# Performance work log

Measured on AMD Instinct MI355X. Metric: run time of the kernel, lower is better.

Reference implementation:

```python
import jax, jax.numpy as jnp
import numpy as np

B, C, H, W = 16, 64, 64, 64
HEADS = 8

def conv1x1(x, w):
    # x: [B, Cin, H, W], w: [Cout, Cin] -> [B, Cout, H, W]
    return jnp.einsum('oc,bchw->bohw', w, x)

def maxpool2x2(x):
    b, c, h, w = x.shape
    return x.reshape(b, c, h // 2, 2, w // 2, 2).max(axis=(3, 5))

def setup_inputs() -> dict:
    key = jax.random.key(0)
    ks = jax.random.split(key, 6)
    x = jax.random.normal(ks[0], (B, C, H, W), dtype=jnp.float32)
    w_theta = jax.random.normal(ks[1], (C // HEADS, C), dtype=jnp.float32) * 0.05
    w_phi = jax.random.normal(ks[2], (C // HEADS, C), dtype=jnp.float32) * 0.05
    w_g = jax.random.normal(ks[3], (C // 2, C), dtype=jnp.float32) * 0.05
    w_o = jax.random.normal(ks[4], (C, C // 2), dtype=jnp.float32) * 0.05
    gamma = jax.random.normal(ks[5], (), dtype=jnp.float32)
    return {'x': x, 'w_theta': w_theta, 'w_phi': w_phi, 'w_g': w_g, 'w_o': w_o, 'gamma': gamma}

def reference(x, w_theta, w_phi, w_g, w_o, gamma):
    b, c, h, w = x.shape
    n = h * w                      # query length
    m = n // 4                     # kv length after 2x2 maxpool
    theta = conv1x1(x, w_theta).reshape(b, c // HEADS, n)   # [B, C/h, N]
    phi = maxpool2x2(conv1x1(x, w_phi)).reshape(b, c // HEADS, m)  # [B, C/h, M]
    g = maxpool2x2(conv1x1(x, w_g)).reshape(b, c // 2, m)   # [B, C/2, M]
    # attention: theta^T @ phi -> [B, N, M]; NOTE: no 1/sqrt(d) scaling (SAGAN)
    beta = jax.nn.softmax(jnp.einsum('bdn,bdm->bnm', theta, phi), axis=-1)
    # o = g @ beta^T -> [B, C/2, N]
    o = jnp.einsum('bdm,bnm->bdn', g, beta).reshape(b, c // 2, h, w)
    o = conv1x1(o, w_o)            # [B, C, H, W]
    return gamma * o + x
```

## Files before the change

kernel.cpp:

```cpp
#include <hip/hip_runtime.h>
#include <hip/hip_bf16.h>

#define NB 16
#define NC 64
#define NN 4096
#define NM 1024
#define ND 8
#define NG 32

typedef short short8 __attribute__((ext_vector_type(8)));
typedef float floatx4 __attribute__((ext_vector_type(4)));
typedef float floatx2 __attribute__((ext_vector_type(2)));

#define LOG2E 1.44269504f

__device__ __forceinline__ short f2bfs(float f) {
    union { __hip_bfloat16 h; short s; } u;
    u.h = __float2bfloat16(f);
    return u.s;
}
__device__ __forceinline__ unsigned pack2bf(float a, float b) {
    return (unsigned)(unsigned short)f2bfs(a) | ((unsigned)(unsigned short)f2bfs(b) << 16);
}
__device__ __forceinline__ unsigned pk2fast(float a, float b) {
    unsigned ua = __float_as_uint(a) + 0x8000u;
    unsigned ub = __float_as_uint(b) + 0x8000u;
    return __builtin_amdgcn_perm(ub, ua, 0x07060302);
}
__device__ __forceinline__ float bflo(unsigned u) { return __uint_as_float(u << 16); }
__device__ __forceinline__ float bfhi(unsigned u) { return __uint_as_float(u & 0xffff0000u); }
__device__ __forceinline__ floatx2 fma2(floatx2 a, float b, floatx2 c) {
    return __builtin_elementwise_fma(a, (floatx2)(b), c);
}

__global__ __launch_bounds__(256)
void proj_kernel(const float* __restrict__ x,
                 const float* __restrict__ w_theta,
                 const float* __restrict__ w_phi,
                 const float* __restrict__ w_g,
                 const float* __restrict__ w_o,
                 unsigned* __restrict__ theta_ws,
                 unsigned* __restrict__ phi_ws,
                 unsigned* __restrict__ g2_ws)
{
    __shared__ __align__(16) float xl[64 * 128];
    __shared__ float lwt[512];
    __shared__ float lwp[512];
    __shared__ float lwg[2048];
    __shared__ float lwo[2048];
    __shared__ __align__(16) float lgs[32 * 36];
    __shared__ float lps[32 * 8];

    const int b  = blockIdx.x >> 5;
    const int ph = blockIdx.x & 31;
    const int t  = threadIdx.x;

    for (int i = t; i < 512;  i += 256) { lwt[i] = w_theta[i]; lwp[i] = w_phi[i]; }
    for (int i = t; i < 2048; i += 256) { lwg[i] = w_g[i];     lwo[i] = w_o[i]; }

    const float* xb = x + (size_t)b * NC * NN + (size_t)ph * 128;
    for (int idx = t; idx < 2048; idx += 256) {
        int c = idx >> 5, i4 = idx & 31;
        ((float4*)xl)[c * 32 + i4] = ((const float4*)(xb + (size_t)c * NN))[i4];
    }
    __syncthreads();

    if (t < 128) {
        float th[8];
        #pragma unroll
        for (int oc = 0; oc < 8; ++oc) th[oc] = 0.f;
        for (int c = 0; c < 64; ++c) {
            float xv = xl[c * 128 + t];
            #pragma unroll
            for (int oc = 0; oc < 8; ++oc) th[oc] = fmaf(lwt[oc * 64 + c], xv, th[oc]);
        }
        uint4 pk;
        pk.x = pack2bf(th[0] * LOG2E, th[1] * LOG2E);
        pk.y = pack2bf(th[2] * LOG2E, th[3] * LOG2E);
        pk.z = pack2bf(th[4] * LOG2E, th[5] * LOG2E);
        pk.w = pack2bf(th[6] * LOG2E, th[7] * LOG2E);
        ((uint4*)theta_ws)[(size_t)b * NN + ph * 128 + t] = pk;

        int m = t >> 2, oc0 = (t & 3) * 2;
        float s[2][4];
        #pragma unroll
        for (int a = 0; a < 2; ++a)
            #pragma unroll
            for (int p = 0; p < 4; ++p) s[a][p] = 0.f;
        #pragma unroll 4
        for (int c = 0; c < 64; ++c) {
            const float* xr = &xl[c * 128];
            float x0 = xr[2 * m], x1 = xr[2 * m + 1], x2 = xr[64 + 2 * m], x3 = xr[65 + 2 * m];
            #pragma unroll
            for (int a = 0; a < 2; ++a) {
                float w = lwp[(oc0 + a) * 64 + c];
                s[a][0] = fmaf(w, x0, s[a][0]);
                s[a][1] = fmaf(w, x1, s[a][1]);
                s[a][2] = fmaf(w, x2, s[a][2]);
                s[a][3] = fmaf(w, x3, s[a][3]);
            }
        }
        #pragma unroll
        for (int a = 0; a < 2; ++a)
            lps[m * 8 + oc0 + a] = fmaxf(fmaxf(s[a][0], s[a][1]), fmaxf(s[a][2], s[a][3]));
    } else {
        int tt = t - 128;
        int oc0 = (tt >> 3) * 2, grp = tt & 7;
        float s0[16], s1[16];
        #pragma unroll
        for (int i = 0; i < 16; ++i) { s0[i] = 0.f; s1[i] = 0.f; }
        const float4* xl4 = (const float4*)xl;
        #pragma unroll 2
        for (int c = 0; c < 64; ++c) {
            float4 a0 = xl4[c * 32 + 2 * grp];
            float4 a1 = xl4[c * 32 + 2 * grp + 1];
            float4 b0 = xl4[c * 32 + 16 + 2 * grp];
            float4 b1 = xl4[c * 32 + 17 + 2 * grp];
            float w0 = lwg[oc0 * 64 + c], w1 = lwg[(oc0 + 1) * 64 + c];
            s0[0] = fmaf(w0, a0.x, s0[0]);  s0[1] = fmaf(w0, a0.y, s0[1]);
            s0[2] = fmaf(w0, a0.z, s0[2]);  s0[3] = fmaf(w0, a0.w, s0[3]);
            s0[4] = fmaf(w0, a1.x, s0[4]);  s0[5] = fmaf(w0, a1.y, s0[5]);
            s0[6] = fmaf(w0, a1.z, s0[6]);  s0[7] = fmaf(w0, a1.w, s0[7]);
            s0[8] = fmaf(w0, b0.x, s0[8]);  s0[9] = fmaf(w0, b0.y, s0[9]);
            s0[10] = fmaf(w0, b0.z, s0[10]); s0[11] = fmaf(w0, b0.w, s0[11]);
            s0[12] = fmaf(w0, b1.x, s0[12]); s0[13] = fmaf(w0, b1.y, s0[13]);
            s0[14] = fmaf(w0, b1.z, s0[14]); s0[15] = fmaf(w0, b1.w, s0[15]);
            s1[0] = fmaf(w1, a0.x, s1[0]);  s1[1] = fmaf(w1, a0.y, s1[1]);
            s1[2] = fmaf(w1, a0.z, s1[2]);  s1[3] = fmaf(w1, a0.w, s1[3]);
            s1[4] = fmaf(w1, a1.x, s1[4]);  s1[5] = fmaf(w1, a1.y, s1[5]);
            s1[6] = fmaf(w1, a1.z, s1[6]);  s1[7] = fmaf(w1, a1.w, s1[7]);
            s1[8] = fmaf(w1, b0.x, s1[8]);  s1[9] = fmaf(w1, b0.y, s1[9]);
            s1[10] = fmaf(w1, b0.z, s1[10]); s1[11] = fmaf(w1, b0.w, s1[11]);
            s1[12] = fmaf(w1, b1.x, s1[12]); s1[13] = fmaf(w1, b1.y, s1[13]);
            s1[14] = fmaf(w1, b1.z, s1[14]); s1[15] = fmaf(w1, b1.w, s1[15]);
        }
        #pragma unroll
        for (int p = 0; p < 4; ++p) {
            float v0 = fmaxf(fmaxf(s0[2 * p], s0[2 * p + 1]), fmaxf(s0[8 + 2 * p], s0[9 + 2 * p]));
            float v1 = fmaxf(fmaxf(s1[2 * p], s1[2 * p + 1]), fmaxf(s1[8 + 2 * p], s1[9 + 2 * p]));
            lgs[oc0 * 36 + grp * 4 + p]       = v0;
            lgs[(oc0 + 1) * 36 + grp * 4 + p] = v1;
        }
    }
    __syncthreads();

    {
        int co = t >> 2, m0 = (t & 3) * 8;
        float v[8];
        #pragma unroll
        for (int mm = 0; mm < 8; ++mm) v[mm] = 0.f;
        #pragma unroll 4
        for (int c = 0; c < 32; ++c) {
            float w = lwo[co * 32 + c];
            float4 ga = ((const float4*)&lgs[c * 36 + m0])[0];
            float4 gb = ((const float4*)&lgs[c * 36 + m0])[1];
            v[0] = fmaf(w, ga.x, v[0]); v[1] = fmaf(w, ga.y, v[1]);
            v[2] = fmaf(w, ga.z, v[2]); v[3] = fmaf(w, ga.w, v[3]);
            v[4] = fmaf(w, gb.x, v[4]); v[5] = fmaf(w, gb.y, v[5]);
            v[6] = fmaf(w, gb.z, v[6]); v[7] = fmaf(w, gb.w, v[7]);
        }
        uint4 pk;
        pk.x = pack2bf(v[0], v[1]); pk.y = pack2bf(v[2], v[3]);
        pk.z = pack2bf(v[4], v[5]); pk.w = pack2bf(v[6], v[7]);
        int lane = ((t & 3) << 4) | ((t >> 2) & 15);
        ((uint4*)g2_ws)[(((size_t)b * 4 + (t >> 6)) * 32 + ph) * 64 + lane] = pk;
    }

    if (t < 32) {
        const float* pr = &lps[t * 8];
        uint4 pk;
        pk.x = pack2bf(pr[0], pr[1]); pk.y = pack2bf(pr[2], pr[3]);
        pk.z = pack2bf(pr[4], pr[5]); pk.w = pack2bf(pr[6], pr[7]);
        ((uint4*)phi_ws)[(size_t)b * NM + ph * 32 + t] = pk;
    }
}

__global__ __launch_bounds__(256, 2)
void attn_kernel(const unsigned* __restrict__ theta_ws,
                 const unsigned* __restrict__ phi_ws,
                 const unsigned* __restrict__ g2_ws,
                 const float* __restrict__ gamma_p,
                 const float* __restrict__ x,
                 float* __restrict__ out)
{
    __shared__ __align__(16) float lphi[NM * 8 + 16];

    const int b    = blockIdx.x >> 5;
    const int qblk = blockIdx.x & 31;
    const int t    = threadIdx.x;
    const int w    = t >> 6;
    const int lane = t & 63;
    const int lm   = lane & 15;
    const int quad = lane >> 4;
    const int q0   = qblk * 128 + w * 32;

    for (int kk = t; kk < NM; kk += 256) {
        uint4 v = ((const uint4*)phi_ws)[(size_t)b * NM + kk];
        float* dst = lphi + kk * 8 + ((kk >> 3) & 3) * 4;
        ((float4*)dst)[0] = make_float4(bflo(v.x), bfhi(v.x), bflo(v.y), bfhi(v.y));
        ((float4*)dst)[1] = make_float4(bflo(v.z), bfhi(v.z), bflo(v.w), bfhi(v.w));
    }

    floatx2 th2[8];
    {
        uint4 v0 = ((const uint4*)theta_ws)[(size_t)b * NN + q0 + lm];
        uint4 v1 = ((const uint4*)theta_ws)[(size_t)b * NN + q0 + 16 + lm];
        th2[0] = floatx2{bflo(v0.x), bflo(v1.x)}; th2[1] = floatx2{bfhi(v0.x), bfhi(v1.x)};
        th2[2] = floatx2{bflo(v0.y), bflo(v1.y)}; th2[3] = floatx2{bfhi(v0.y), bfhi(v1.y)};
        th2[4] = floatx2{bflo(v0.z), bflo(v1.z)}; th2[5] = floatx2{bfhi(v0.z), bfhi(v1.z)};
        th2[6] = floatx2{bflo(v0.w), bflo(v1.w)}; th2[7] = floatx2{bfhi(v0.w), bfhi(v1.w)};
    }

    floatx4 acc[2][4];
    #pragma unroll
    for (int qt = 0; qt < 2; ++qt)
        #pragma unroll
        for (int ct = 0; ct < 4; ++ct) acc[qt][ct] = (floatx4)0.f;
    floatx2 lsum2 = (floatx2)0.f;

    const uint4* gf = (const uint4*)g2_ws;
    uint4 ga[4], gn[4];
    #pragma unroll
    for (int ct = 0; ct < 4; ++ct)
        ga[ct] = gf[(((size_t)b * 4 + ct) * 32 + 0) * 64 + lane];

    __syncthreads();

    for (int kg = 0; kg < 32; ++kg) {
        if (kg + 1 < 32) {
            #pragma unroll
            for (int ct = 0; ct < 4; ++ct)
                gn[ct] = gf[(((size_t)b * 4 + ct) * 32 + kg + 1) * 64 + lane];
        }
        const float* pb = lphi + kg * 256 + quad * 68;
        floatx2 p2[8];
        #pragma unroll
        for (int j = 0; j < 8; ++j) {
            float4 f0 = ((const float4*)(pb + j * 8))[0];
            float4 f1 = ((const float4*)(pb + j * 8))[1];
            floatx2 s2 = th2[0] * f0.x;
            s2 = fma2(th2[1], f0.y, s2); s2 = fma2(th2[2], f0.z, s2);
            s2 = fma2(th2[3], f0.w, s2); s2 = fma2(th2[4], f1.x, s2);
            s2 = fma2(th2[5], f1.y, s2); s2 = fma2(th2[6], f1.z, s2);
            s2 = fma2(th2[7], f1.w, s2);
            floatx2 e2;
            e2.x = exp2f(s2.x);
            e2.y = exp2f(s2.y);
            lsum2 += e2;
            p2[j] = e2;
        }
        union { unsigned u[4]; short8 s; } pf0, pf1;
        #pragma unroll
        for (int jj = 0; jj < 4; ++jj) {
            pf0.u[jj] = pk2fast(p2[2 * jj].x, p2[2 * jj + 1].x);
            pf1.u[jj] = pk2fast(p2[2 * jj].y, p2[2 * jj + 1].y);
        }
        #pragma unroll
        for (int ct = 0; ct < 4; ++ct) {
            union { uint4 v; short8 s; } a;
            a.v = ga[ct];
            acc[0][ct] = __builtin_amdgcn_mfma_f32_16x16x32_bf16(a.s, pf0.s, acc[0][ct], 0, 0, 0);
            acc[1][ct] = __builtin_amdgcn_mfma_f32_16x16x32_bf16(a.s, pf1.s, acc[1][ct], 0, 0, 0);
        }
        #pragma unroll
        for (int ct = 0; ct < 4; ++ct) ga[ct] = gn[ct];
    }

    float inv[2];
    {
        float l0 = lsum2.x; l0 += __shfl_xor(l0, 16); l0 += __shfl_xor(l0, 32);
        float l1 = lsum2.y; l1 += __shfl_xor(l1, 16); l1 += __shfl_xor(l1, 32);
        inv[0] = 1.0f / l0; inv[1] = 1.0f / l1;
    }

    const float gamma = gamma_p[0];
    #pragma unroll
    for (int qt = 0; qt < 2; ++qt) {
        const int q = q0 + qt * 16 + lm;
        #pragma unroll
        for (int ct = 0; ct < 4; ++ct) {
            #pragma unroll
            for (int r = 0; r < 4; ++r) {
                int co = ct * 16 + quad * 4 + r;
                size_t idx = ((size_t)b * NC + co) * NN + q;
                out[idx] = fmaf(gamma, acc[qt][ct][r] * inv[qt], x[idx]);
            }
        }
    }
}

extern "C" void kernel_launch(void* const* d_in, const int* in_sizes, int n_in,
                              void* d_out, int out_size, void* d_ws, size_t ws_size,
                              hipStream_t stream)
{
    const float* x  = (const float*)d_in[0];
    const float* wt = (const float*)d_in[1];
    const float* wp = (const float*)d_in[2];
    const float* wg = (const float*)d_in[3];
    const float* wo = (const float*)d_in[4];
    const float* gm = (const float*)d_in[5];
    float* out = (float*)d_out;

    unsigned* theta_ws = (unsigned*)d_ws;
    unsigned* phi_ws   = theta_ws + (size_t)NB * NN * ND / 2;
    unsigned* g2_ws    = phi_ws   + (size_t)NB * NM * ND / 2;

    proj_kernel<<<NB * 32, 256, 0, stream>>>(x, wt, wp, wg, wo, theta_ws, phi_ws, g2_ws);
    attn_kernel<<<NB * 32, 256, 0, stream>>>(theta_ws, phi_ws, g2_ws, gm, x, out);
}
```

Before: 128.5 us.

## Compute attention scores with MFMA instead of scalar FMA on unpacked phi

The QK^T score computation moves from packed fp32 FMAs over a float-expanded phi tile in LDS to bf16 MFMA instructions, with theta zero-padded to fill the 32-wide K dimension. Phi now stays as packed bf16 in LDS and is prefetched one key group ahead in registers, and the g layout written by the projection kernel is reordered to match the new P-operand layout. This removes the VALU-bound dot products and the LDS unpack, but wastes MFMA work on zero padding and doubles the PV MFMA count because of half-filled operands.

```diff
diff --git a/kernel.cpp b/kernel.cpp
--- a/kernel.cpp
+++ b/kernel.cpp
@@ -10,7 +10,6 @@
 
 typedef short short8 __attribute__((ext_vector_type(8)));
 typedef float floatx4 __attribute__((ext_vector_type(4)));
-typedef float floatx2 __attribute__((ext_vector_type(2)));
 
 #define LOG2E 1.44269504f
 
@@ -27,10 +26,8 @@
     unsigned ub = __float_as_uint(b) + 0x8000u;
     return __builtin_amdgcn_perm(ub, ua, 0x07060302);
 }
-__device__ __forceinline__ float bflo(unsigned u) { return __uint_as_float(u << 16); }
-__device__ __forceinline__ float bfhi(unsigned u) { return __uint_as_float(u & 0xffff0000u); }
-__device__ __forceinline__ floatx2 fma2(floatx2 a, float b, floatx2 c) {
-    return __builtin_elementwise_fma(a, (floatx2)(b), c);
+__device__ __forceinline__ short8 u4s8(uint4 v) {
+    union { uint4 u; short8 s; } c; c.u = v; return c.s;
 }
 
 __global__ __launch_bounds__(256)
@@ -145,15 +142,16 @@
     __syncthreads();
 
     {
-        int co = t >> 2, m0 = (t & 3) * 8;
+        int co = t >> 2, sel = t & 3;
+        int m0a = 4 * sel, m0b = 16 + 4 * sel;
         float v[8];
         #pragma unroll
         for (int mm = 0; mm < 8; ++mm) v[mm] = 0.f;
         #pragma unroll 4
         for (int c = 0; c < 32; ++c) {
             float w = lwo[co * 32 + c];
-            float4 ga = ((const float4*)&lgs[c * 36 + m0])[0];
-            float4 gb = ((const float4*)&lgs[c * 36 + m0])[1];
+            float4 ga = *(const float4*)&lgs[c * 36 + m0a];
+            float4 gb = *(const float4*)&lgs[c * 36 + m0b];
             v[0] = fmaf(w, ga.x, v[0]); v[1] = fmaf(w, ga.y, v[1]);
             v[2] = fmaf(w, ga.z, v[2]); v[3] = fmaf(w, ga.w, v[3]);
             v[4] = fmaf(w, gb.x, v[4]); v[5] = fmaf(w, gb.y, v[5]);
@@ -162,8 +160,8 @@
         uint4 pk;
         pk.x = pack2bf(v[0], v[1]); pk.y = pack2bf(v[2], v[3]);
         pk.z = pack2bf(v[4], v[5]); pk.w = pack2bf(v[6], v[7]);
-        int lane = ((t & 3) << 4) | ((t >> 2) & 15);
-        ((uint4*)g2_ws)[(((size_t)b * 4 + (t >> 6)) * 32 + ph) * 64 + lane] = pk;
+        int lane = (sel << 4) | (co & 15);
+        ((uint4*)g2_ws)[(((size_t)b * 4 + (co >> 4)) * 32 + ph) * 64 + lane] = pk;
     }
 
     if (t < 32) {
@@ -183,7 +181,7 @@
                  const float* __restrict__ x,
                  float* __restrict__ out)
 {
-    __shared__ __align__(16) float lphi[NM * 8 + 16];
+    __shared__ __align__(16) uint4 lphi[NM];
 
     const int b    = blockIdx.x >> 5;
     const int qblk = blockIdx.x & 31;
@@ -194,21 +192,17 @@
     const int quad = lane >> 4;
     const int q0   = qblk * 128 + w * 32;
 
-    for (int kk = t; kk < NM; kk += 256) {
-        uint4 v = ((const uint4*)phi_ws)[(size_t)b * NM + kk];
-        float* dst = lphi + kk * 8 + ((kk >> 3) & 3) * 4;
-        ((float4*)dst)[0] = make_float4(bflo(v.x), bfhi(v.x), bflo(v.y), bfhi(v.y));
-        ((float4*)dst)[1] = make_float4(bflo(v.z), bfhi(v.z), bflo(v.w), bfhi(v.w));
-    }
-
-    floatx2 th2[8];
-    {
-        uint4 v0 = ((const uint4*)theta_ws)[(size_t)b * NN + q0 + lm];
-        uint4 v1 = ((const uint4*)theta_ws)[(size_t)b * NN + q0 + 16 + lm];
-        th2[0] = floatx2{bflo(v0.x), bflo(v1.x)}; th2[1] = floatx2{bfhi(v0.x), bfhi(v1.x)};
-        th2[2] = floatx2{bflo(v0.y), bflo(v1.y)}; th2[3] = floatx2{bfhi(v0.y), bfhi(v1.y)};
-        th2[4] = floatx2{bflo(v0.z), bflo(v1.z)}; th2[5] = floatx2{bfhi(v0.z), bfhi(v1.z)};
-        th2[6] = floatx2{bflo(v0.w), bflo(v1.w)}; th2[7] = floatx2{bfhi(v0.w), bfhi(v1.w)};
+    for (int kk = t; kk < NM; kk += 256)
+        lphi[kk] = ((const uint4*)phi_ws)[(size_t)b * NM + kk];
+
+    uint4 tb[2];
+    #pragma unroll
+    for (int qt = 0; qt < 2; ++qt) {
+        uint4 v = ((const uint4*)theta_ws)[(size_t)b * NN + q0 + qt * 16 + lm];
+        tb[qt].x = quad == 0 ? v.x : 0u;
+        tb[qt].y = quad == 0 ? v.y : 0u;
+        tb[qt].z = quad == 0 ? v.z : 0u;
+        tb[qt].w = quad == 0 ? v.w : 0u;
     }
 
     floatx4 acc[2][4];
@@ -216,7 +210,7 @@
     for (int qt = 0; qt < 2; ++qt)
         #pragma unroll
         for (int ct = 0; ct < 4; ++ct) acc[qt][ct] = (floatx4)0.f;
-    floatx2 lsum2 = (floatx2)0.f;
+    float lsum[2] = {0.f, 0.f};
 
     const uint4* gf = (const uint4*)g2_ws;
     uint4 ga[4], gn[4];
@@ -226,50 +220,52 @@
 
     __syncthreads();
 
+    uint4 pp0 = lphi[lm];
+    uint4 pp1 = lphi[16 + lm];
+
     for (int kg = 0; kg < 32; ++kg) {
         if (kg + 1 < 32) {
             #pragma unroll
             for (int ct = 0; ct < 4; ++ct)
                 gn[ct] = gf[(((size_t)b * 4 + ct) * 32 + kg + 1) * 64 + lane];
         }
-        const float* pb = lphi + kg * 256 + quad * 68;
-        floatx2 p2[8];
-        #pragma unroll
-        for (int j = 0; j < 8; ++j) {
-            float4 f0 = ((const float4*)(pb + j * 8))[0];
-            float4 f1 = ((const float4*)(pb + j * 8))[1];
-            floatx2 s2 = th2[0] * f0.x;
-            s2 = fma2(th2[1], f0.y, s2); s2 = fma2(th2[2], f0.z, s2);
-            s2 = fma2(th2[3], f0.w, s2); s2 = fma2(th2[4], f1.x, s2);
-            s2 = fma2(th2[5], f1.y, s2); s2 = fma2(th2[6], f1.z, s2);
-            s2 = fma2(th2[7], f1.w, s2);
-            floatx2 e2;
-            e2.x = exp2f(s2.x);
-            e2.y = exp2f(s2.y);
-            lsum2 += e2;
-            p2[j] = e2;
-        }
-        union { unsigned u[4]; short8 s; } pf0, pf1;
-        #pragma unroll
-        for (int jj = 0; jj < 4; ++jj) {
-            pf0.u[jj] = pk2fast(p2[2 * jj].x, p2[2 * jj + 1].x);
-            pf1.u[jj] = pk2fast(p2[2 * jj].y, p2[2 * jj + 1].y);
-        }
-        #pragma unroll
-        for (int ct = 0; ct < 4; ++ct) {
-            union { uint4 v; short8 s; } a;
-            a.v = ga[ct];
-            acc[0][ct] = __builtin_amdgcn_mfma_f32_16x16x32_bf16(a.s, pf0.s, acc[0][ct], 0, 0, 0);
-            acc[1][ct] = __builtin_amdgcn_mfma_f32_16x16x32_bf16(a.s, pf1.s, acc[1][ct], 0, 0, 0);
+        uint4 pn0, pn1;
+        if (kg + 1 < 32) {
+            pn0 = lphi[(kg + 1) * 32 + lm];
+            pn1 = lphi[(kg + 1) * 32 + 16 + lm];
+        }
+
+        #pragma unroll
+        for (int qt = 0; qt < 2; ++qt) {
+            floatx4 s0 = __builtin_amdgcn_mfma_f32_16x16x32_bf16(
+                u4s8(pp0), u4s8(tb[qt]), (floatx4)0.f, 0, 0, 0);
+            floatx4 s1 = __builtin_amdgcn_mfma_f32_16x16x32_bf16(
+                u4s8(pp1), u4s8(tb[qt]), (floatx4)0.f, 0, 0, 0);
+            float e0[4], e1[4];
+            #pragma unroll
+            for (int r = 0; r < 4; ++r) { e0[r] = exp2f(s0[r]); e1[r] = exp2f(s1[r]); }
+            lsum[qt] += ((e0[0] + e0[1]) + (e0[2] + e0[3]))
+                      + ((e1[0] + e1[1]) + (e1[2] + e1[3]));
+            uint4 pb0 = make_uint4(pk2fast(e0[0], e0[1]), pk2fast(e0[2], e0[3]), 0u, 0u);
+            uint4 pb1 = make_uint4(pk2fast(e1[0], e1[1]), pk2fast(e1[2], e1[3]), 0u, 0u);
+            #pragma unroll
+            for (int ct = 0; ct < 4; ++ct) {
+                acc[qt][ct] = __builtin_amdgcn_mfma_f32_16x16x32_bf16(
+                    u4s8(ga[ct]), u4s8(pb0), acc[qt][ct], 0, 0, 0);
+                uint4 a1 = make_uint4(ga[ct].z, ga[ct].w, ga[ct].z, ga[ct].w);
+                acc[qt][ct] = __builtin_amdgcn_mfma_f32_16x16x32_bf16(
+                    u4s8(a1), u4s8(pb1), acc[qt][ct], 0, 0, 0);
+            }
         }
         #pragma unroll
         for (int ct = 0; ct < 4; ++ct) ga[ct] = gn[ct];
+        pp0 = pn0; pp1 = pn1;
     }
 
     float inv[2];
     {
-        float l0 = lsum2.x; l0 += __shfl_xor(l0, 16); l0 += __shfl_xor(l0, 32);
-        float l1 = lsum2.y; l1 += __shfl_xor(l1, 16); l1 += __shfl_xor(l1, 32);
+        float l0 = lsum[0]; l0 += __shfl_xor(l0, 16); l0 += __shfl_xor(l0, 32);
+        float l1 = lsum[1]; l1 += __shfl_xor(l1, 16); l1 += __shfl_xor(l1, 32);
         inv[0] = 1.0f / l0; inv[1] = 1.0f / l1;
     }
 
```

After: 121.2 us. 5.7% less time.
